# Performance work log

Hardware: AMD Instinct MI355X
Metric: run time of the kernel (lower is better)

The kernel has to match this reference:

```python
import jax, jax.numpy as jnp
import numpy as np

B, F, U, O, A, H = 8192, 1024, 512, 3, 6, 4  # batch, features, nb_units, nb_opponents, actions, heads
HD = U // H  # head dim


def setup_inputs() -> dict:
    key = jax.random.key(0)
    ks = jax.random.split(key, 12)
    s = 0.02
    rn = lambda k, shape: jax.random.normal(k, shape, jnp.float32) * s
    return {
        "features": jax.random.normal(ks[0], (B, F), jnp.float32),
        # agent latent Linear
        "W_al": rn(ks[1], (U, F)), "b_al": jnp.zeros((U,), jnp.float32),
        # MultiheadAttention in_proj (q,k,v stacked) and out_proj
        "W_in": rn(ks[2], (3 * U, U)), "b_in": jnp.zeros((3 * U,), jnp.float32),
        "W_out": rn(ks[3], (U, U)), "b_out": jnp.zeros((U,), jnp.float32),
        # agent head / policy / value
        "W_ah": rn(ks[4], (U, 2 * U)), "b_ah": jnp.zeros((U,), jnp.float32),
        "W_ap": rn(ks[5], (A, U)), "b_ap": jnp.zeros((A,), jnp.float32),
        "W_av": rn(ks[6], (1, U)), "b_av": jnp.zeros((1,), jnp.float32),
        # per-opponent stacks: latent, head, policy, value
        "W_ol": rn(ks[7], (O, U, F)), "b_ol": jnp.zeros((O, U), jnp.float32),
        "W_oh": rn(ks[8], (O, U, U)), "b_oh": jnp.zeros((O, U), jnp.float32),
        "W_op": rn(ks[9], (O, A, U)), "b_op": jnp.zeros((O, A), jnp.float32),
        "W_ov": rn(ks[10], (O, 1, U)), "b_ov": jnp.zeros((O, 1), jnp.float32),
    }


def reference(features, W_al, b_al, W_in, b_in, W_out, b_out, W_ah, b_ah,
              W_ap, b_ap, W_av, b_av, W_ol, b_ol, W_oh, b_oh, W_op, b_op, W_ov, b_ov):
    elu = jax.nn.elu
    # agent + per-opponent latents (per-opponent linears as one grouped GEMM)
    agent_latent = elu(features @ W_al.T + b_al)                                # [B,U]
    opp_lat = elu(jnp.einsum('bf,ouf->obu', features, W_ol) + b_ol[:, None, :])  # [O,B,U]

    # torch.nn.MultiheadAttention: query=[1,B,U] (agent), key=value=[O,B,U] (opponents)
    Wq, Wk, Wv = W_in[:U], W_in[U:2 * U], W_in[2 * U:]
    bq, bk, bv = b_in[:U], b_in[U:2 * U], b_in[2 * U:]
    q = (agent_latent @ Wq.T + bq).reshape(B, H, HD) * (1.0 / np.sqrt(HD))      # [B,H,HD]
    k = (jnp.einsum('obu,vu->obv', opp_lat, Wk) + bk).reshape(O, B, H, HD)
    v = (jnp.einsum('obu,vu->obv', opp_lat, Wv) + bv).reshape(O, B, H, HD)
    scores = jnp.einsum('bhd,obhd->bho', q, k)                                  # [B,H,O]
    w = jax.nn.softmax(scores, axis=-1)
    attn = jnp.einsum('bho,obhd->bhd', w, v).reshape(B, U)
    attn_out = attn @ W_out.T + b_out                                           # [B,U]
    opponents_influences = w.mean(axis=1)                                       # [B,O] (avg over heads)

    # agent head / policy / value
    cat = jnp.concatenate([agent_latent, attn_out], axis=1)                     # [B,2U]
    agent_head = elu(cat @ W_ah.T + b_ah)
    agent_policy = agent_head @ W_ap.T + b_ap                                   # [B,A]
    agent_value = agent_head @ W_av.T + b_av                                    # [B,1]

    # per-opponent head / policy / value (grouped GEMMs)
    opp_heads = elu(jnp.einsum('obu,ovu->obv', opp_lat, W_oh) + b_oh[:, None, :])  # [O,B,U]
    opponents_policies = jnp.einsum('obu,oau->boa', opp_heads, W_op) + b_op[None]   # [B,O,A]
    opponents_values = jnp.einsum('obu,ocu->boc', opp_heads, W_ov) + b_ov[None]     # [B,O,1]

    return (agent_policy, agent_value, opponents_policies, opponents_values, opponents_influences)
```

## Files before the change

### kernel.cpp

```cpp
#include <hip/hip_runtime.h>

typedef unsigned short u16;
typedef __bf16 bf16x8 __attribute__((ext_vector_type(8)));
typedef float f32x4 __attribute__((ext_vector_type(4)));

#define Bsz 8192
#define Fdim 1024
#define Udim 512
#define Odim 3
#define Adim 6
#define Hdim 4

#define OFF_FEAT   0
#define OFF_WAL    8388608
#define OFF_WIN    8912896
#define OFF_WOUT   9699328
#define OFF_WAH    9961472
#define OFF_WOL    10485760
#define OFF_WOH    12058624
#define OFF_CAT    12845056
#define OFF_OPP    21233664
#define OFF_Q      33816576
#define OFF_KV     38010880
#define OFF_ATT    63176704
#define OFF_AGH    67371008
#define OFF_OPH    71565312

#define OUT_AP 0
#define OUT_AV 49152
#define OUT_OP 57344
#define OUT_OV 204800
#define OUT_IN 229376

__device__ __forceinline__ u16 f2bf(float f) {
  return __builtin_bit_cast(u16, (__bf16)f);
}
__device__ __forceinline__ float bf2f(u16 u) {
  return (float)__builtin_bit_cast(__bf16, u);
}

__device__ __forceinline__ void gload16(const u16* g, u16* s) {
  __builtin_amdgcn_global_load_lds(
      (const __attribute__((address_space(1))) unsigned int*)g,
      (__attribute__((address_space(3))) unsigned int*)s, 16, 0, 0);
}

#define CV_E0 2097152
#define CV_E1 2228224
#define CV_E2 2424832
#define CV_E3 2490368
#define CV_E4 2621440
#define CV_E5 3014656
#define CV_E6 3211264
__global__ __launch_bounds__(256) void convert_all(
    const float* __restrict__ f, const float* __restrict__ wal,
    const float* __restrict__ win, const float* __restrict__ wout,
    const float* __restrict__ wah, const float* __restrict__ wol,
    const float* __restrict__ woh, u16* __restrict__ dst) {
  int i = blockIdx.x * 256 + threadIdx.x;
  if (i >= CV_E6) return;
  const float* src;
  int base;
  if (i < CV_E0)      { src = f;    base = 0; }
  else if (i < CV_E1) { src = wal;  base = CV_E0; }
  else if (i < CV_E2) { src = win;  base = CV_E1; }
  else if (i < CV_E3) { src = wout; base = CV_E2; }
  else if (i < CV_E4) { src = wah;  base = CV_E3; }
  else if (i < CV_E5) { src = wol;  base = CV_E4; }
  else                { src = woh;  base = CV_E5; }
  float4 v = ((const float4*)src)[i - base];
  ushort4 o;
  o.x = f2bf(v.x); o.y = f2bf(v.y); o.z = f2bf(v.z); o.w = f2bf(v.w);
  ((ushort4*)dst)[i] = o;
}

template <int BN, bool ELU>
__global__ __launch_bounds__(256) void gemm_bt(
    const u16* __restrict__ A, const u16* __restrict__ Bw, u16* __restrict__ C,
    const float* __restrict__ bias, int K, int lda, int ldb, int ldc,
    long sAz, long sBz, long sCz, int sbz, float scale) {
  constexpr int BM = 128, BK = 32;
  constexpr int NI = BN / 32;
  __shared__ __align__(16) u16 As[BM * BK];
  __shared__ __align__(16) u16 Bs[BN * BK];
  const int wave = threadIdx.x >> 6, lane = threadIdx.x & 63;

  const int nx = gridDim.x, ny = gridDim.y;
  const int nxy = nx * ny;
  const int nwg = nxy * gridDim.z;
  const int orig = blockIdx.x + nx * (blockIdx.y + ny * blockIdx.z);
  const int xcd = orig & 7;
  const int qd = nwg >> 3, rd = nwg & 7;
  const int wg = (xcd < rd ? xcd * (qd + 1) : rd * (qd + 1) + (xcd - rd) * qd)
               + (orig >> 3);
  const int z = wg / nxy;
  const int rem = wg - z * nxy;
  const int by = rem / nx;
  const int bx = rem - by * nx;

  A += (size_t)z * sAz;
  Bw += (size_t)z * sBz;
  C += (size_t)z * sCz;
  bias += (size_t)z * sbz;
  const int tM = by * BM, tN = bx * BN;
  const int wr = wave >> 1, wc = wave & 1;

  f32x4 acc[4][NI];
#pragma unroll
  for (int i = 0; i < 4; i++)
#pragma unroll
    for (int j = 0; j < NI; j++) acc[i][j] = (f32x4){0.f, 0.f, 0.f, 0.f};

  const int srow = lane >> 2;
  const int scol = (lane & 3) * 8;

  for (int k0 = 0; k0 < K; k0 += BK) {
    __syncthreads();
#pragma unroll
    for (int i = 0; i < 2; ++i) {
      int r = wave * 32 + i * 16;
      gload16(A + (size_t)(tM + r + srow) * lda + k0 + scol, &As[r * BK]);
    }
#pragma unroll
    for (int i = 0; i < BN / 64; ++i) {
      int r = (wave * (BN / 64) + i) * 16;
      gload16(Bw + (size_t)(tN + r + srow) * ldb + k0 + scol, &Bs[r * BK]);
    }
    __syncthreads();
    bf16x8 af[4], bfr[NI];
#pragma unroll
    for (int mi = 0; mi < 4; mi++)
      af[mi] = *(const bf16x8*)&As[(wr * 64 + mi * 16 + (lane & 15)) * BK + (lane >> 4) * 8];
#pragma unroll
    for (int ni = 0; ni < NI; ni++)
      bfr[ni] = *(const bf16x8*)&Bs[(wc * (BN / 2) + ni * 16 + (lane & 15)) * BK + (lane >> 4) * 8];
#pragma unroll
    for (int mi = 0; mi < 4; mi++)
#pragma unroll
      for (int ni = 0; ni < NI; ni++)
        acc[mi][ni] = __builtin_amdgcn_mfma_f32_16x16x32_bf16(af[mi], bfr[ni], acc[mi][ni], 0, 0, 0);
  }

#pragma unroll
  for (int ni = 0; ni < NI; ni++) {
    int col = tN + wc * (BN / 2) + ni * 16 + (lane & 15);
    float bv = bias[col];
#pragma unroll
    for (int mi = 0; mi < 4; mi++) {
      int row0 = tM + wr * 64 + mi * 16 + (lane >> 4) * 4;
#pragma unroll
      for (int r = 0; r < 4; r++) {
        float v = (acc[mi][ni][r] + bv) * scale;
        if (ELU) v = v > 0.f ? v : (__expf(v) - 1.f);
        C[(size_t)(row0 + r) * ldc + col] = f2bf(v);
      }
    }
  }
}

__global__ __launch_bounds__(256) void attn_kernel(
    const u16* __restrict__ q, const u16* __restrict__ kv,
    u16* __restrict__ attn, float* __restrict__ influ) {
  const int wave = threadIdx.x >> 6, lane = threadIdx.x & 63;
  const int b = blockIdx.x * 4 + wave;
  const size_t qb = (size_t)b * 512;
  float wacc0 = 0.f, wacc1 = 0.f, wacc2 = 0.f;
#pragma unroll
  for (int h = 0; h < 4; ++h) {
    const int off = h * 128 + lane * 2;
    ushort2 qu = *(const ushort2*)(q + qb + off);
    float qx = bf2f(qu.x), qy = bf2f(qu.y);
    float s[3];
#pragma unroll
    for (int o = 0; o < 3; ++o) {
      ushort2 ku = *(const ushort2*)(kv + (size_t)o * (Bsz * 1024) + (size_t)b * 1024 + off);
      float p = qx * bf2f(ku.x) + qy * bf2f(ku.y);
#pragma unroll
      for (int d = 32; d; d >>= 1) p += __shfl_xor(p, d, 64);
      s[o] = p;
    }
    float m = fmaxf(s[0], fmaxf(s[1], s[2]));
    float e0 = __expf(s[0] - m), e1 = __expf(s[1] - m), e2 = __expf(s[2] - m);
    float inv = 1.f / (e0 + e1 + e2);
    float w0 = e0 * inv, w1 = e1 * inv, w2 = e2 * inv;
    wacc0 += w0; wacc1 += w1; wacc2 += w2;
    float ax = 0.f, ay = 0.f;
#pragma unroll
    for (int o = 0; o < 3; ++o) {
      float w = (o == 0) ? w0 : (o == 1) ? w1 : w2;
      ushort2 vu = *(const ushort2*)(kv + (size_t)o * (Bsz * 1024) + (size_t)b * 1024 + 512 + off);
      ax += w * bf2f(vu.x);
      ay += w * bf2f(vu.y);
    }
    ushort2 st; st.x = f2bf(ax); st.y = f2bf(ay);
    *(ushort2*)(attn + qb + off) = st;
  }
  if (lane == 0) {
    influ[b * 3 + 0] = wacc0 * 0.25f;
    influ[b * 3 + 1] = wacc1 * 0.25f;
    influ[b * 3 + 2] = wacc2 * 0.25f;
  }
}

__global__ __launch_bounds__(256) void heads_kernel(
    const u16* __restrict__ ah, const u16* __restrict__ oh,
    const float* __restrict__ Wap, const float* __restrict__ bap,
    const float* __restrict__ Wav, const float* __restrict__ bav,
    const float* __restrict__ Wop, const float* __restrict__ bop,
    const float* __restrict__ Wov, const float* __restrict__ bov,
    float* __restrict__ out) {
  __shared__ float sW[14336];
  for (int i = threadIdx.x; i < 14336; i += 256) {
    int s = i / 3584, rem = i - s * 3584;
    float v;
    if (s == 0) {
      v = (rem < 3072) ? Wap[rem] : Wav[rem - 3072];
    } else {
      int o = s - 1;
      v = (rem < 3072) ? Wop[o * 3072 + rem] : Wov[o * 512 + (rem - 3072)];
    }
    sW[i] = v;
  }
  __syncthreads();
  const int wave = threadIdx.x >> 6, lane = threadIdx.x & 63;
  const int kq = lane & 7, r = lane >> 3;
  const int b = blockIdx.x * 32 + wave * 8 + r;

  const u16* srcs[4] = {ah + (size_t)b * 512,
                        oh + (size_t)b * 512,
                        oh + (size_t)(Bsz + b) * 512,
                        oh + (size_t)(2 * Bsz + b) * 512};
  bf16x8 a[4][8];
#pragma unroll
  for (int s = 0; s < 4; s++)
#pragma unroll
    for (int c = 0; c < 8; c++)
      a[s][c] = *(const bf16x8*)(srcs[s] + c * 64 + kq * 8);

#pragma unroll
  for (int s = 0; s < 4; s++) {
#pragma unroll
    for (int p = 0; p < 7; p++) {
      const float* w = &sW[s * 3584 + p * 512 + kq * 8];
      float acc = 0.f;
#pragma unroll
      for (int c = 0; c < 8; c++) {
#pragma unroll
        for (int j = 0; j < 8; j++)
          acc += (float)a[s][c][j] * w[c * 64 + j];
      }
      acc += __shfl_xor(acc, 1, 64);
      acc += __shfl_xor(acc, 2, 64);
      acc += __shfl_xor(acc, 4, 64);
      if (kq == p) {
        if (s == 0) {
          if (p < 6) out[OUT_AP + b * 6 + p] = acc + bap[p];
          else       out[OUT_AV + b] = acc + bav[0];
        } else {
          int o = s - 1;
          if (p < 6) out[OUT_OP + b * 18 + o * 6 + p] = acc + bop[o * 6 + p];
          else       out[OUT_OV + b * 3 + o] = acc + bov[o];
        }
      }
    }
  }
}

extern "C" void kernel_launch(void* const* d_in, const int* in_sizes, int n_in,
                              void* d_out, int out_size, void* d_ws, size_t ws_size,
                              hipStream_t stream) {
  (void)in_sizes; (void)n_in; (void)out_size; (void)ws_size;
  const float* f     = (const float*)d_in[0];
  const float* W_al  = (const float*)d_in[1];
  const float* b_al  = (const float*)d_in[2];
  const float* W_in  = (const float*)d_in[3];
  const float* b_in  = (const float*)d_in[4];
  const float* W_out = (const float*)d_in[5];
  const float* b_out = (const float*)d_in[6];
  const float* W_ah  = (const float*)d_in[7];
  const float* b_ah  = (const float*)d_in[8];
  const float* W_ap  = (const float*)d_in[9];
  const float* b_ap  = (const float*)d_in[10];
  const float* W_av  = (const float*)d_in[11];
  const float* b_av  = (const float*)d_in[12];
  const float* W_ol  = (const float*)d_in[13];
  const float* b_ol  = (const float*)d_in[14];
  const float* W_oh  = (const float*)d_in[15];
  const float* b_oh  = (const float*)d_in[16];
  const float* W_op  = (const float*)d_in[17];
  const float* b_op  = (const float*)d_in[18];
  const float* W_ov  = (const float*)d_in[19];
  const float* b_ov  = (const float*)d_in[20];
  float* out = (float*)d_out;
  u16* ws = (u16*)d_ws;

  u16* feat = ws + OFF_FEAT;
  u16* wal  = ws + OFF_WAL;
  u16* win  = ws + OFF_WIN;
  u16* wout = ws + OFF_WOUT;
  u16* wah  = ws + OFF_WAH;
  u16* wol  = ws + OFF_WOL;
  u16* woh  = ws + OFF_WOH;
  u16* cat  = ws + OFF_CAT;
  u16* opp  = ws + OFF_OPP;
  u16* qb   = ws + OFF_Q;
  u16* kvb  = ws + OFF_KV;
  u16* att  = ws + OFF_ATT;
  u16* agh  = ws + OFF_AGH;
  u16* oph  = ws + OFF_OPH;

  convert_all<<<12544, 256, 0, stream>>>(f, W_al, W_in, W_out, W_ah, W_ol, W_oh, ws);

  gemm_bt<64, true><<<dim3(8, 64, 1), 256, 0, stream>>>(
      feat, wal, cat, b_al, 1024, 1024, 1024, 1024, 0, 0, 0, 0, 1.f);
  gemm_bt<128, true><<<dim3(12, 64, 1), 256, 0, stream>>>(
      feat, wol, opp, b_ol, 1024, 1024, 1024, 1536, 0, 0, 0, 0, 1.f);
  gemm_bt<64, false><<<dim3(8, 64, 1), 256, 0, stream>>>(
      cat, win, qb, b_in, 512, 1024, 512, 512, 0, 0, 0, 0, 0.08838834764831845f);
  gemm_bt<128, false><<<dim3(8, 64, 3), 256, 0, stream>>>(
      opp, win + 262144, kvb, b_in + 512, 512, 1536, 512, 1024, 512, 0, 8388608, 0, 1.f);

  attn_kernel<<<2048, 256, 0, stream>>>(qb, kvb, att, out + OUT_IN);

  gemm_bt<64, false><<<dim3(8, 64, 1), 256, 0, stream>>>(
      att, wout, cat + 512, b_out, 512, 512, 512, 1024, 0, 0, 0, 0, 1.f);
  gemm_bt<64, true><<<dim3(8, 64, 1), 256, 0, stream>>>(
      cat, wah, agh, b_ah, 1024, 1024, 1024, 512, 0, 0, 0, 0, 1.f);
  gemm_bt<128, true><<<dim3(4, 64, 3), 256, 0, stream>>>(
      opp, woh, oph, b_oh, 512, 1536, 512, 512, 512, 262144, 4194304, 512, 1.f);

  heads_kernel<<<256, 256, 0, stream>>>(agh, oph, W_ap, b_ap, W_av, b_av,
                                        W_op, b_op, W_ov, b_ov, out);
}
```

Baseline: 330.5 us.

## Fuse latent GEMMs and add 256x256 double-buffered GEMM for big projections

Reorders the weight workspace so W_al and W_ol sit next to each other, then computes the agent and opponent latents in one GEMM with N=2048 and a split bias. That GEMM and the K/V projection move to a new 256x256-tile kernel with 512 threads, double-buffered LDS, a swizzled LDS layout, and interleaved MFMA/load phases using setprio. The concat buffer goes away: gemm_bt gains a second A pointer with a K split, so the agent-head GEMM reads the latent and attention-output buffers directly. The new kernel uses about 128KB of LDS per block and assumes dimensions are multiples of 256.

```diff
diff --git a/kernel.cpp b/kernel.cpp
--- a/kernel.cpp
+++ b/kernel.cpp
@@ -13,16 +13,16 @@
 
 #define OFF_FEAT   0
 #define OFF_WAL    8388608
-#define OFF_WIN    8912896
-#define OFF_WOUT   9699328
-#define OFF_WAH    9961472
-#define OFF_WOL    10485760
+#define OFF_WOL    8912896
+#define OFF_WIN    10485760
+#define OFF_WOUT   11272192
+#define OFF_WAH    11534336
 #define OFF_WOH    12058624
-#define OFF_CAT    12845056
-#define OFF_OPP    21233664
-#define OFF_Q      33816576
-#define OFF_KV     38010880
-#define OFF_ATT    63176704
+#define OFF_LAT    12845056
+#define OFF_Q      29622272
+#define OFF_KV     33816576
+#define OFF_ATT    58982400
+#define OFF_AOUT   63176704
 #define OFF_AGH    67371008
 #define OFF_OPH    71565312
 
@@ -47,15 +47,15 @@
 
 #define CV_E0 2097152
 #define CV_E1 2228224
-#define CV_E2 2424832
-#define CV_E3 2490368
-#define CV_E4 2621440
+#define CV_E2 2621440
+#define CV_E3 2818048
+#define CV_E4 2883584
 #define CV_E5 3014656
 #define CV_E6 3211264
 __global__ __launch_bounds__(256) void convert_all(
     const float* __restrict__ f, const float* __restrict__ wal,
-    const float* __restrict__ win, const float* __restrict__ wout,
-    const float* __restrict__ wah, const float* __restrict__ wol,
+    const float* __restrict__ wol, const float* __restrict__ win,
+    const float* __restrict__ wout, const float* __restrict__ wah,
     const float* __restrict__ woh, u16* __restrict__ dst) {
   int i = blockIdx.x * 256 + threadIdx.x;
   if (i >= CV_E6) return;
@@ -63,10 +63,10 @@
   int base;
   if (i < CV_E0)      { src = f;    base = 0; }
   else if (i < CV_E1) { src = wal;  base = CV_E0; }
-  else if (i < CV_E2) { src = win;  base = CV_E1; }
-  else if (i < CV_E3) { src = wout; base = CV_E2; }
-  else if (i < CV_E4) { src = wah;  base = CV_E3; }
-  else if (i < CV_E5) { src = wol;  base = CV_E4; }
+  else if (i < CV_E2) { src = wol;  base = CV_E1; }
+  else if (i < CV_E3) { src = win;  base = CV_E2; }
+  else if (i < CV_E4) { src = wout; base = CV_E3; }
+  else if (i < CV_E5) { src = wah;  base = CV_E4; }
   else                { src = woh;  base = CV_E5; }
   float4 v = ((const float4*)src)[i - base];
   ushort4 o;
@@ -74,16 +74,48 @@
   ((ushort4*)dst)[i] = o;
 }
 
-template <int BN, bool ELU>
-__global__ __launch_bounds__(256) void gemm_bt(
+#define BAR() __builtin_amdgcn_s_barrier()
+#define FENCE() asm volatile("" ::: "memory")
+#define LGKM0() asm volatile("s_waitcnt lgkmcnt(0)" ::: "memory")
+#define VMW(n) asm volatile("s_waitcnt vmcnt(" #n ")" ::: "memory")
+#define STAGE(MAT, SRC, LD, buf, ks, kb) do {                    \
+    const u16* _s = (SRC) + (size_t)(kb) + (ks) * 32;            \
+    gload16(_s, &MAT[buf][ks][wave * 512]);                      \
+    gload16(_s + (size_t)128 * (LD), &MAT[buf][ks][4096 + wave * 512]); \
+  } while (0)
+#define RD_A(cur, ks, mh) do {                                   \
+    _Pragma("unroll")                                            \
+    for (int mi = 0; mi < 4; mi++)                               \
+      a0[mi] = *(const bf16x8*)&As[cur][ks][aoff + (mh)*2048 + mi*512]; \
+  } while (0)
+#define RD_B(cur, ks) do {                                       \
+    _Pragma("unroll")                                            \
+    for (int ni = 0; ni < 4; ni++)                               \
+      b0[ni] = *(const bf16x8*)&Bs[cur][ks][boff + ni*512];      \
+  } while (0)
+#define MFMA8(mh) do {                                           \
+    __builtin_amdgcn_s_setprio(1);                               \
+    _Pragma("unroll")                                            \
+    for (int mi = 0; mi < 4; mi++) {                             \
+      _Pragma("unroll")                                          \
+      for (int ni = 0; ni < 4; ni++)                             \
+        acc[(mh)*4+mi][ni] = __builtin_amdgcn_mfma_f32_16x16x32_bf16( \
+            a0[mi], b0[ni], acc[(mh)*4+mi][ni], 0, 0, 0);        \
+    }                                                            \
+    __builtin_amdgcn_s_setprio(0);                               \
+  } while (0)
+
+template <bool ELU>
+__global__ __launch_bounds__(512, 2) void gemm256(
     const u16* __restrict__ A, const u16* __restrict__ Bw, u16* __restrict__ C,
-    const float* __restrict__ bias, int K, int lda, int ldb, int ldc,
+    const float* __restrict__ bias1, const float* __restrict__ bias2,
+    int bsplit, int K, int lda, int ldb, int ldc,
     long sAz, long sBz, long sCz, int sbz, float scale) {
-  constexpr int BM = 128, BK = 32;
-  constexpr int NI = BN / 32;
-  __shared__ __align__(16) u16 As[BM * BK];
-  __shared__ __align__(16) u16 Bs[BN * BK];
-  const int wave = threadIdx.x >> 6, lane = threadIdx.x & 63;
+  __shared__ __align__(16) u16 As[2][2][8192];
+  __shared__ __align__(16) u16 Bs[2][2][8192];
+  const int tid = threadIdx.x;
+  const int wave = tid >> 6, lane = tid & 63;
+  const int wr = wave >> 2, wc = wave & 3;
 
   const int nx = gridDim.x, ny = gridDim.y;
   const int nxy = nx * ny;
@@ -101,6 +133,117 @@
   A += (size_t)z * sAz;
   Bw += (size_t)z * sBz;
   C += (size_t)z * sCz;
+  bias1 += (size_t)z * sbz;
+
+  const int tM = by * 256, tN = bx * 256;
+
+  const int srow = tid >> 2;
+  const int schunk = ((tid & 3) ^ ((tid >> 3) & 3)) * 8;
+  const u16* Asrc = A + (size_t)(tM + srow) * lda + schunk;
+  const u16* Bsrc = Bw + (size_t)(tN + srow) * ldb + schunk;
+
+  const int laneLo = lane & 15;
+  const int pc8 = (((lane >> 4) ^ ((lane >> 1) & 3))) * 8;
+  const int aoff = (wr * 128 + laneLo) * 32 + pc8;
+  const int boff = (wc * 64 + laneLo) * 32 + pc8;
+
+  f32x4 acc[8][4];
+#pragma unroll
+  for (int mi = 0; mi < 8; mi++)
+#pragma unroll
+    for (int ni = 0; ni < 4; ni++) acc[mi][ni] = (f32x4){0.f, 0.f, 0.f, 0.f};
+
+  const int NT = K >> 6;
+
+  STAGE(As, Asrc, lda, 0, 0, 0);
+  STAGE(Bs, Bsrc, ldb, 0, 0, 0);
+  STAGE(As, Asrc, lda, 0, 1, 0);
+  STAGE(Bs, Bsrc, ldb, 0, 1, 0);
+  VMW(4);
+  BAR();
+
+  int cur = 0;
+  int kb = 64;
+  bf16x8 a0[4], b0[4];
+  for (int t = 0; t < NT; ++t) {
+    const int nxt = cur ^ 1;
+    const bool st = (t + 1 < NT);
+    RD_B(cur, 0);
+    RD_A(cur, 0, 0);
+    if (st) STAGE(As, Asrc, lda, nxt, 0, kb);
+    FENCE(); BAR(); LGKM0();
+    MFMA8(0);
+    FENCE(); BAR();
+    RD_A(cur, 0, 1);
+    if (st) STAGE(Bs, Bsrc, ldb, nxt, 0, kb);
+    FENCE(); BAR(); LGKM0();
+    MFMA8(1);
+    if (st) { VMW(4); } else { VMW(0); }
+    BAR();
+    RD_B(cur, 1);
+    RD_A(cur, 1, 0);
+    if (st) STAGE(As, Asrc, lda, nxt, 1, kb);
+    FENCE(); BAR(); LGKM0();
+    MFMA8(0);
+    FENCE(); BAR();
+    RD_A(cur, 1, 1);
+    if (st) STAGE(Bs, Bsrc, ldb, nxt, 1, kb);
+    FENCE(); BAR(); LGKM0();
+    MFMA8(1);
+    if (st) { VMW(4); BAR(); }
+    cur = nxt;
+    kb += 64;
+  }
+
+#pragma unroll
+  for (int ni = 0; ni < 4; ni++) {
+    const int col = tN + wc * 64 + ni * 16 + laneLo;
+    const float bv = (col < bsplit) ? bias1[col] : bias2[col - bsplit];
+#pragma unroll
+    for (int gm = 0; gm < 8; gm++) {
+      const int row0 = tM + wr * 128 + gm * 16 + (lane >> 4) * 4;
+#pragma unroll
+      for (int r = 0; r < 4; r++) {
+        float v = (acc[gm][ni][r] + bv) * scale;
+        if (ELU) v = v > 0.f ? v : (__expf(v) - 1.f);
+        C[(size_t)(row0 + r) * ldc + col] = f2bf(v);
+      }
+    }
+  }
+}
+#undef STAGE
+#undef RD_A
+#undef RD_B
+#undef MFMA8
+
+template <int BN, bool ELU>
+__global__ __launch_bounds__(256) void gemm_bt(
+    const u16* __restrict__ A, const u16* __restrict__ A2, int ksplit, int lda2,
+    const u16* __restrict__ Bw, u16* __restrict__ C,
+    const float* __restrict__ bias, int K, int lda, int ldb, int ldc,
+    long sAz, long sBz, long sCz, int sbz, float scale) {
+  constexpr int BM = 128, BK = 32;
+  constexpr int NI = BN / 32;
+  __shared__ __align__(16) u16 As[BM * BK];
+  __shared__ __align__(16) u16 Bs[BN * BK];
+  const int wave = threadIdx.x >> 6, lane = threadIdx.x & 63;
+
+  const int nx = gridDim.x, ny = gridDim.y;
+  const int nxy = nx * ny;
+  const int nwg = nxy * gridDim.z;
+  const int orig = blockIdx.x + nx * (blockIdx.y + ny * blockIdx.z);
+  const int xcd = orig & 7;
+  const int qd = nwg >> 3, rd = nwg & 7;
+  const int wg = (xcd < rd ? xcd * (qd + 1) : rd * (qd + 1) + (xcd - rd) * qd)
+               + (orig >> 3);
+  const int z = wg / nxy;
+  const int rem = wg - z * nxy;
+  const int by = rem / nx;
+  const int bx = rem - by * nx;
+
+  A += (size_t)z * sAz;
+  Bw += (size_t)z * sBz;
+  C += (size_t)z * sCz;
   bias += (size_t)z * sbz;
   const int tM = by * BM, tN = bx * BN;
   const int wr = wave >> 1, wc = wave & 1;
@@ -115,11 +258,15 @@
   const int scol = (lane & 3) * 8;
 
   for (int k0 = 0; k0 < K; k0 += BK) {
+    const u16* Ap;
+    int la, kk;
+    if (k0 < ksplit) { Ap = A;  la = lda;  kk = k0; }
+    else             { Ap = A2; la = lda2; kk = k0 - ksplit; }
     __syncthreads();
 #pragma unroll
     for (int i = 0; i < 2; ++i) {
       int r = wave * 32 + i * 16;
-      gload16(A + (size_t)(tM + r + srow) * lda + k0 + scol, &As[r * BK]);
+      gload16(Ap + (size_t)(tM + r + srow) * la + kk + scol, &As[r * BK]);
     }
 #pragma unroll
     for (int i = 0; i < BN / 64; ++i) {
@@ -299,35 +446,38 @@
   u16* win  = ws + OFF_WIN;
   u16* wout = ws + OFF_WOUT;
   u16* wah  = ws + OFF_WAH;
-  u16* wol  = ws + OFF_WOL;
   u16* woh  = ws + OFF_WOH;
-  u16* cat  = ws + OFF_CAT;
-  u16* opp  = ws + OFF_OPP;
+  u16* lat  = ws + OFF_LAT;
   u16* qb   = ws + OFF_Q;
   u16* kvb  = ws + OFF_KV;
   u16* att  = ws + OFF_ATT;
+  u16* aout = ws + OFF_AOUT;
   u16* agh  = ws + OFF_AGH;
   u16* oph  = ws + OFF_OPH;
 
-  convert_all<<<12544, 256, 0, stream>>>(f, W_al, W_in, W_out, W_ah, W_ol, W_oh, ws);
-
+  convert_all<<<12544, 256, 0, stream>>>(f, W_al, W_ol, W_in, W_out, W_ah,
+                                         W_oh, ws);
+
+  gemm256<true><<<dim3(8, 32, 1), 512, 0, stream>>>(
+      feat, wal, lat, b_al, b_ol, 512, 1024, 1024, 1024, 2048, 0, 0, 0, 0, 1.f);
+  gemm_bt<64, false><<<dim3(8, 64, 1), 256, 0, stream>>>(
+      lat, lat, 1 << 30, 2048, win, qb, b_in, 512, 2048, 512, 512,
+      0, 0, 0, 0, 0.08838834764831845f);
+  gemm256<false><<<dim3(4, 32, 3), 512, 0, stream>>>(
+      lat + 512, win + 262144, kvb, b_in + 512, b_in + 512, 1 << 30,
+      512, 2048, 512, 1024, 512, 0, 8388608, 0, 1.f);
+
+  attn_kernel<<<2048, 256, 0, stream>>>(qb, kvb, att, out + OUT_IN);
+
+  gemm_bt<64, false><<<dim3(8, 64, 1), 256, 0, stream>>>(
+      att, att, 1 << 30, 512, wout, aout, b_out, 512, 512, 512, 512,
+      0, 0, 0, 0, 1.f);
   gemm_bt<64, true><<<dim3(8, 64, 1), 256, 0, stream>>>(
-      feat, wal, cat, b_al, 1024, 1024, 1024, 1024, 0, 0, 0, 0, 1.f);
-  gemm_bt<128, true><<<dim3(12, 64, 1), 256, 0, stream>>>(
-      feat, wol, opp, b_ol, 1024, 1024, 1024, 1536, 0, 0, 0, 0, 1.f);
-  gemm_bt<64, false><<<dim3(8, 64, 1), 256, 0, stream>>>(
-      cat, win, qb, b_in, 512, 1024, 512, 512, 0, 0, 0, 0, 0.08838834764831845f);
-  gemm_bt<128, false><<<dim3(8, 64, 3), 256, 0, stream>>>(
-      opp, win + 262144, kvb, b_in + 512, 512, 1536, 512, 1024, 512, 0, 8388608, 0, 1.f);
-
-  attn_kernel<<<2048, 256, 0, stream>>>(qb, kvb, att, out + OUT_IN);
-
-  gemm_bt<64, false><<<dim3(8, 64, 1), 256, 0, stream>>>(
-      att, wout, cat + 512, b_out, 512, 512, 512, 1024, 0, 0, 0, 0, 1.f);
-  gemm_bt<64, true><<<dim3(8, 64, 1), 256, 0, stream>>>(
-      cat, wah, agh, b_ah, 1024, 1024, 1024, 512, 0, 0, 0, 0, 1.f);
+      lat, aout, 512, 512, wah, agh, b_ah, 1024, 2048, 1024, 512,
+      0, 0, 0, 0, 1.f);
   gemm_bt<128, true><<<dim3(4, 64, 3), 256, 0, stream>>>(
-      opp, woh, oph, b_oh, 512, 1536, 512, 512, 512, 262144, 4194304, 512, 1.f);
+      lat + 512, lat + 512, 1 << 30, 2048, woh, oph, b_oh, 512, 2048, 512, 512,
+      512, 262144, 4194304, 512, 1.f);
 
   heads_kernel<<<256, 256, 0, stream>>>(agh, oph, W_ap, b_ap, W_av, b_av,
                                         W_op, b_op, W_ov, b_ov, out);
```

Result: no change. 324.6 us (-1.8%).
